# Optimization experiments

Hardware: AMD Instinct MI355X
Metric: run time of the kernel (lower is better)

## Reference

```python
import jax, jax.numpy as jnp
import numpy as np

P_THRESH = 20  # p=0.2 * 100
# direction -> (di, dj): masked pixel (i,j) writes input[i,j] to x[i+di, j+dj], then avg to x[i,j]
OFFSETS = {0: (-1, -1), 1: (-1, 0), 2: (-1, 1), 3: (0, -1), 4: (0, 0), 5: (0, 1), 6: (1, -1), 7: (1, 0)}


def _shift(a, di, dj):
    """out[i+di, j+dj] = a[i, j] on last two axes; out-of-range -> 0/False."""
    H, W = a.shape[-2], a.shape[-1]
    pad = [(0, 0)] * (a.ndim - 2) + [(max(di, 0), max(-di, 0)), (max(dj, 0), max(-dj, 0))]
    p = jnp.pad(a, pad)
    sh, sw = max(-di, 0), max(-dj, 0)
    return p[..., sh:sh + H, sw:sw + W]


def _avg3x3_reflect(x):
    H, W = x.shape[-2], x.shape[-1]
    p = jnp.pad(x, [(0, 0), (0, 0), (1, 1), (1, 1)], mode='reflect')
    s = jnp.zeros_like(x)
    for i in range(3):
        for j in range(3):
            s = s + p[..., i:i + H, j:j + W]
    return s / 9.0


def brown_forward(input, dir, prob):
    avg = _avg3x3_reflect(input)
    pos = prob <= P_THRESH
    x = input
    for d in range(8):  # sequential, matching torch in-place write order
        di, dj = OFFSETS[d]
        m = (dir == d) & pos
        if d == 4:
            x = jnp.where(m, avg, x)  # mm: only avg write
        else:
            sm = _shift(m, di, dj)                       # neighbor-target mask
            x = jnp.where(sm, _shift(input, di, dj), x)  # x[i+di,j+dj] = input[i,j]
            mv = _shift(sm, -di, -dj)                    # mask restricted to valid region
            x = jnp.where(mv, avg, x)                    # x[i,j] = avg[i,j]
    return x


def setup_inputs() -> dict:
    key = jax.random.key(0)
    k1, k2, k3 = jax.random.split(key, 3)
    shape = (32, 64, 128, 128)
    return {
        'input': jax.random.normal(k1, shape, dtype=jnp.float32),
        'dir': jax.random.randint(k2, shape, 0, 8, dtype=jnp.int32),
        'prob': jax.random.randint(k3, shape, 1, 100, dtype=jnp.int32),
    }


def reference(input, dir, prob):
    return brown_forward(input, dir, prob)
```

## Files before the change

### kernel.cpp

```cpp
#include <hip/hip_runtime.h>
#include <cstddef>

#define H 128
#define W 128
#define TILE_R 32
#define LROWS (TILE_R + 2)
#define P_THRESH 20

__global__ __launch_bounds__(256, 4)
void brown_kernel(const float* __restrict__ inp,
                  const int*  __restrict__ dirp,
                  const int*  __restrict__ prb,
                  float* __restrict__ out)
{
    __shared__ float s_in[LROWS * W];
    __shared__ int   s_mk[LROWS * W];

    const int tid   = threadIdx.x;
    const int bid   = blockIdx.x;
    const int slice = bid >> 2;
    const int r0    = (bid & 3) * TILE_R;
    const size_t base = (size_t)slice * (size_t)(H * W);

    for (int idx = tid; idx < LROWS * (W / 4); idx += 256) {
        const int L  = idx >> 5;
        const int c4 = idx & 31;
        const int gr = r0 - 1 + L;
        const int gri = (gr < 0) ? 1 : ((gr >= H) ? (H - 2) : gr);
        const float4 iv = ((const float4*)(inp + base + (size_t)gri * W))[c4];
        ((float4*)(s_in + L * W))[c4] = iv;
        int4 mv;
        if (gr >= 0 && gr < H) {
            const int4 dv = ((const int4*)(dirp + base + (size_t)gr * W))[c4];
            const int4 pv = ((const int4*)(prb  + base + (size_t)gr * W))[c4];
            mv.x = (pv.x <= P_THRESH) ? dv.x : 8;
            mv.y = (pv.y <= P_THRESH) ? dv.y : 8;
            mv.z = (pv.z <= P_THRESH) ? dv.z : 8;
            mv.w = (pv.w <= P_THRESH) ? dv.w : 8;
        } else {
            mv = make_int4(8, 8, 8, 8);
        }
        ((int4*)(s_mk + L * W))[c4] = mv;
    }
    __syncthreads();

    for (int k = 0; k < 4; ++k) {
        const int item = k * 256 + tid;
        const int lr = item >> 5;
        const int cq = item & 31;
        const int j0 = cq << 2;
        const int gi = r0 + lr;

        float v[3][6];
        int   m[3][6];
        #pragma unroll
        for (int r = 0; r < 3; ++r) {
            const int Lr = lr + r;
            const float4 c  = ((const float4*)(s_in + Lr * W))[cq];
            const int4   mc = ((const int4*)(s_mk + Lr * W))[cq];
            v[r][1] = c.x;  v[r][2] = c.y;  v[r][3] = c.z;  v[r][4] = c.w;
            m[r][1] = mc.x; m[r][2] = mc.y; m[r][3] = mc.z; m[r][4] = mc.w;
            const float lf = s_in[Lr * W + j0 - 1];
            const int   ml = s_mk[Lr * W + j0 - 1];
            const float rt = s_in[Lr * W + j0 + 4];
            const int   mr = s_mk[Lr * W + j0 + 4];
            v[r][0] = (cq > 0)  ? lf : c.y;
            m[r][0] = (cq > 0)  ? ml : 8;
            v[r][5] = (cq < 31) ? rt : c.z;
            m[r][5] = (cq < 31) ? mr : 8;
        }

        float cs[6];
        #pragma unroll
        for (int w = 0; w < 6; ++w) cs[w] = v[0][w] + v[1][w] + v[2][w];

        float4 res;
        float* rp = (float*)&res;
        #pragma unroll
        for (int p = 0; p < 4; ++p) {
            const float avg = (cs[p] + cs[p + 1] + cs[p + 2]) * (1.0f / 9.0f);
            float val = v[1][p + 1];
            int dl = -1;

            if (m[2][p + 2] == 0) { val = v[2][p + 2]; dl = 0; }
            if (m[2][p + 1] == 1) { val = v[2][p + 1]; dl = 1; }
            if (m[2][p]     == 2) { val = v[2][p];     dl = 2; }
            if (m[1][p + 2] == 3) { val = v[1][p + 2]; dl = 3; }
            if (m[1][p]     == 5) { val = v[1][p];     dl = 5; }
            if (m[0][p + 2] == 6) { val = v[0][p + 2]; dl = 6; }
            if (m[0][p + 1] == 7) { val = v[0][p + 1]; dl = 7; }

            const int msel = m[1][p + 1];
            const int gj = j0 + p;
            const int q3 = msel / 3;
            const int di = q3 - 1;
            const int dj = msel - q3 * 3 - 1;
            const int ti = gi + di;
            const int tj = gj + dj;
            const bool bok = (msel < 8) & (ti >= 0) & (ti < H) & (tj >= 0) & (tj < W);
            if (bok & (msel >= dl)) val = avg;
            rp[p] = val;
        }
        ((float4*)(out + base + (size_t)gi * W))[cq] = res;
    }
}

extern "C" void kernel_launch(void* const* d_in, const int* in_sizes, int n_in,
                              void* d_out, int out_size, void* d_ws, size_t ws_size,
                              hipStream_t stream) {
    const float* inp  = (const float*)d_in[0];
    const int*   dirp = (const int*)d_in[1];
    const int*   prb  = (const int*)d_in[2];
    float* out = (float*)d_out;

    const int slices = in_sizes[0] / (H * W);
    const int grid = slices * (H / TILE_R);
    brown_kernel<<<grid, 256, 0, stream>>>(inp, dirp, prb, out);
}
```

Before: 398.7 us.

## Pack masks to bytes, load input via direct global-to-LDS, slide rows in registers

```diff
diff --git a/kernel.cpp b/kernel.cpp
--- a/kernel.cpp
+++ b/kernel.cpp
@@ -7,14 +7,17 @@
 #define LROWS (TILE_R + 2)
 #define P_THRESH 20
 
-__global__ __launch_bounds__(256, 4)
+typedef __attribute__((address_space(1))) const unsigned int glo_u32;
+typedef __attribute__((address_space(3))) unsigned int lds_u32;
+
+__global__ __launch_bounds__(256, 6)
 void brown_kernel(const float* __restrict__ inp,
                   const int*  __restrict__ dirp,
                   const int*  __restrict__ prb,
                   float* __restrict__ out)
 {
-    __shared__ float s_in[LROWS * W];
-    __shared__ int   s_mk[LROWS * W];
+    __shared__ float        s_in[LROWS * W];
+    __shared__ unsigned int s_mk[LROWS * 32];
 
     const int tid   = threadIdx.x;
     const int bid   = blockIdx.x;
@@ -22,86 +25,104 @@
     const int r0    = (bid & 3) * TILE_R;
     const size_t base = (size_t)slice * (size_t)(H * W);
 
-    for (int idx = tid; idx < LROWS * (W / 4); idx += 256) {
-        const int L  = idx >> 5;
-        const int c4 = idx & 31;
-        const int gr = r0 - 1 + L;
-        const int gri = (gr < 0) ? 1 : ((gr >= H) ? (H - 2) : gr);
-        const float4 iv = ((const float4*)(inp + base + (size_t)gri * W))[c4];
-        ((float4*)(s_in + L * W))[c4] = iv;
-        int4 mv;
-        if (gr >= 0 && gr < H) {
-            const int4 dv = ((const int4*)(dirp + base + (size_t)gr * W))[c4];
-            const int4 pv = ((const int4*)(prb  + base + (size_t)gr * W))[c4];
-            mv.x = (pv.x <= P_THRESH) ? dv.x : 8;
-            mv.y = (pv.y <= P_THRESH) ? dv.y : 8;
-            mv.z = (pv.z <= P_THRESH) ? dv.z : 8;
-            mv.w = (pv.w <= P_THRESH) ? dv.w : 8;
-        } else {
-            mv = make_int4(8, 8, 8, 8);
+    #pragma unroll
+    for (int i = 0; i < 5; ++i) {
+        const int idx = i * 256 + tid;
+        if (idx < LROWS * 32) {
+            const int L  = idx >> 5;
+            const int c4 = idx & 31;
+            const int gr = r0 - 1 + L;
+            const int gri = (gr < 0) ? 1 : ((gr >= H) ? (H - 2) : gr);
+            const float* gp = inp + base + (size_t)gri * W + c4 * 4;
+            __builtin_amdgcn_global_load_lds((glo_u32*)gp, (lds_u32*)(s_in + idx * 4), 16, 0, 0);
+            unsigned m;
+            if (gr >= 0 && gr < H) {
+                const int4 dv = ((const int4*)(dirp + base + (size_t)gr * W))[c4];
+                const int4 pv = ((const int4*)(prb  + base + (size_t)gr * W))[c4];
+                const unsigned a = (pv.x <= P_THRESH) ? (unsigned)dv.x : 8u;
+                const unsigned b = (pv.y <= P_THRESH) ? (unsigned)dv.y : 8u;
+                const unsigned c = (pv.z <= P_THRESH) ? (unsigned)dv.z : 8u;
+                const unsigned d = (pv.w <= P_THRESH) ? (unsigned)dv.w : 8u;
+                m = a | (b << 8) | (c << 16) | (d << 24);
+            } else {
+                m = 0x08080808u;
+            }
+            s_mk[idx] = m;
         }
-        ((int4*)(s_mk + L * W))[c4] = mv;
     }
     __syncthreads();
 
-    for (int k = 0; k < 4; ++k) {
-        const int item = k * 256 + tid;
-        const int lr = item >> 5;
-        const int cq = item & 31;
-        const int j0 = cq << 2;
-        const int gi = r0 + lr;
+    const int cq  = tid & 31;
+    const int rg  = tid >> 5;
+    const int j0  = cq << 2;
+    const int lrb = rg << 2;
+    const int cqm1 = (cq > 0)  ? cq - 1 : 0;
+    const int cqp1 = (cq < 31) ? cq + 1 : 31;
 
-        float v[3][6];
-        int   m[3][6];
-        #pragma unroll
-        for (int r = 0; r < 3; ++r) {
-            const int Lr = lr + r;
-            const float4 c  = ((const float4*)(s_in + Lr * W))[cq];
-            const int4   mc = ((const int4*)(s_mk + Lr * W))[cq];
-            v[r][1] = c.x;  v[r][2] = c.y;  v[r][3] = c.z;  v[r][4] = c.w;
-            m[r][1] = mc.x; m[r][2] = mc.y; m[r][3] = mc.z; m[r][4] = mc.w;
-            const float lf = s_in[Lr * W + j0 - 1];
-            const int   ml = s_mk[Lr * W + j0 - 1];
-            const float rt = s_in[Lr * W + j0 + 4];
-            const int   mr = s_mk[Lr * W + j0 + 4];
-            v[r][0] = (cq > 0)  ? lf : c.y;
-            m[r][0] = (cq > 0)  ? ml : 8;
-            v[r][5] = (cq < 31) ? rt : c.z;
-            m[r][5] = (cq < 31) ? mr : 8;
-        }
+    auto load_row = [&](int Lr, float v[6], unsigned& ma, unsigned& mb) {
+        const float4 c      = ((const float4*)(s_in + Lr * W))[cq];
+        const unsigned mwc  = s_mk[Lr * 32 + cq];
+        const unsigned mwl  = s_mk[Lr * 32 + cqm1];
+        const unsigned mwr  = s_mk[Lr * 32 + cqp1];
+        const float lf = __shfl_up(c.w, 1);
+        const float rt = __shfl_down(c.x, 1);
+        v[1] = c.x; v[2] = c.y; v[3] = c.z; v[4] = c.w;
+        v[0] = (cq > 0)  ? lf : c.y;
+        v[5] = (cq < 31) ? rt : c.z;
+        const unsigned ml = (cq > 0)  ? (mwl >> 24)   : 8u;
+        const unsigned mr = (cq < 31) ? (mwr & 255u)  : 8u;
+        ma = (mwc << 8) | ml;
+        mb = (mwc >> 8) | (mr << 24);
+    };
 
+    float va[6], vb[6], vc[6];
+    unsigned maa, mab, mba, mbb, mca, mcb;
+    load_row(lrb + 0, va, maa, mab);
+    load_row(lrb + 1, vb, mba, mbb);
+
+    #pragma unroll
+    for (int rr = 0; rr < 4; ++rr) {
+        load_row(lrb + rr + 2, vc, mca, mcb);
+
+        const int gi = r0 + lrb + rr;
         float cs[6];
         #pragma unroll
-        for (int w = 0; w < 6; ++w) cs[w] = v[0][w] + v[1][w] + v[2][w];
+        for (int w = 0; w < 6; ++w) cs[w] = va[w] + vb[w] + vc[w];
 
         float4 res;
         float* rp = (float*)&res;
         #pragma unroll
         for (int p = 0; p < 4; ++p) {
             const float avg = (cs[p] + cs[p + 1] + cs[p + 2]) * (1.0f / 9.0f);
-            float val = v[1][p + 1];
+            const unsigned wTop = (p < 2) ? (maa >> (8 * p)) : (mab >> (8 * (p - 2)));
+            const unsigned wMid = (p < 2) ? (mba >> (8 * p)) : (mbb >> (8 * (p - 2)));
+            const unsigned wBot = (p < 2) ? (mca >> (8 * p)) : (mcb >> (8 * (p - 2)));
+
+            float val = vb[p + 1];
             int dl = -1;
+            if (((wBot >> 16) & 255u) == 0u) { val = vc[p + 2]; dl = 0; }
+            if (((wBot >>  8) & 255u) == 1u) { val = vc[p + 1]; dl = 1; }
+            if (( wBot        & 255u) == 2u) { val = vc[p];     dl = 2; }
+            if (((wMid >> 16) & 255u) == 3u) { val = vb[p + 2]; dl = 3; }
+            if (( wMid        & 255u) == 5u) { val = vb[p];     dl = 5; }
+            if (((wTop >> 16) & 255u) == 6u) { val = va[p + 2]; dl = 6; }
+            if (((wTop >>  8) & 255u) == 7u) { val = va[p + 1]; dl = 7; }
 
-            if (m[2][p + 2] == 0) { val = v[2][p + 2]; dl = 0; }
-            if (m[2][p + 1] == 1) { val = v[2][p + 1]; dl = 1; }
-            if (m[2][p]     == 2) { val = v[2][p];     dl = 2; }
-            if (m[1][p + 2] == 3) { val = v[1][p + 2]; dl = 3; }
-            if (m[1][p]     == 5) { val = v[1][p];     dl = 5; }
-            if (m[0][p + 2] == 6) { val = v[0][p + 2]; dl = 6; }
-            if (m[0][p + 1] == 7) { val = v[0][p + 1]; dl = 7; }
-
-            const int msel = m[1][p + 1];
-            const int gj = j0 + p;
-            const int q3 = msel / 3;
+            const int msel = (int)((wMid >> 8) & 255u);
+            const int q3 = (msel * 11) >> 5;
             const int di = q3 - 1;
             const int dj = msel - q3 * 3 - 1;
             const int ti = gi + di;
-            const int tj = gj + dj;
-            const bool bok = (msel < 8) & (ti >= 0) & (ti < H) & (tj >= 0) & (tj < W);
+            const int tj = j0 + p + dj;
+            const bool bok = (msel < 8) & ((unsigned)ti < 128u) & ((unsigned)tj < 128u);
             if (bok & (msel >= dl)) val = avg;
             rp[p] = val;
         }
         ((float4*)(out + base + (size_t)gi * W))[cq] = res;
+
+        #pragma unroll
+        for (int w = 0; w < 6; ++w) { va[w] = vb[w]; vb[w] = vc[w]; }
+        maa = mba; mab = mbb; mba = mca; mbb = mcb;
     }
 }
 
```

After: 388.0 us. -2.7%, faster.
